# Performance work log

Measured on AMD Instinct MI355X. Metric: run time of the kernel, lower is better.

## Reference

```python
import jax, jax.numpy as jnp
import numpy as np

EPS = 1e-5
CHUNK = 512  # chunk of known points for the running-argmin 1-NN search


def nn_idx(unknown, known):
    """1-NN index of each unknown point into known. unknown (B,n,3), known (B,m,3) -> (B,n) int32."""
    B, n, _ = unknown.shape
    m = known.shape[1]
    u2 = jnp.sum(unknown * unknown, axis=-1)  # (B,n)
    # (num_chunks, B, CHUNK, 3)
    kc = known.reshape(B, m // CHUNK, CHUNK, 3).transpose(1, 0, 2, 3)

    def step(carry, kch):
        best_d, best_i, off = carry
        k2 = jnp.sum(kch * kch, axis=-1)  # (B,CHUNK)
        # squared distances for this chunk: (B,n,CHUNK)
        d = u2[:, :, None] - 2.0 * jnp.einsum('bnd,bcd->bnc', unknown, kch) + k2[:, None, :]
        dmin = jnp.min(d, axis=-1)
        imin = jnp.argmin(d, axis=-1).astype(jnp.int32) + off
        upd = dmin < best_d
        return (jnp.where(upd, dmin, best_d), jnp.where(upd, imin, best_i), off + CHUNK), None

    init = (jnp.full((B, n), jnp.inf, unknown.dtype),
            jnp.zeros((B, n), jnp.int32),
            jnp.int32(0))
    (_, best_i, _), _ = jax.lax.scan(step, init, kc)
    return best_i


def bn_relu(x, gamma, beta):
    """Training-mode BatchNorm over (B, n) per channel followed by ReLU. x: (B,C,n)."""
    mean = jnp.mean(x, axis=(0, 2), keepdims=True)
    var = jnp.mean(jnp.square(x - mean), axis=(0, 2), keepdims=True)  # biased, as torch BN
    y = (x - mean) * jax.lax.rsqrt(var + EPS)
    return jax.nn.relu(y * gamma[None, :, None] + beta[None, :, None])


def setup_inputs() -> dict:
    key = jax.random.key(0)
    ks = jax.random.split(key, 8)
    B, n, m, C1, C2 = 2, 65536, 16384, 128, 256
    mlp = [C2 + C1, 256, 128]
    return {
        'unknown': jax.random.normal(ks[0], (B, n, 3), jnp.float32),
        'known': jax.random.normal(ks[1], (B, m, 3), jnp.float32),
        'unknow_feats': jax.random.normal(ks[2], (B, C1, n), jnp.float32),
        'known_feats': jax.random.normal(ks[3], (B, C2, m), jnp.float32),
        'w1': jax.random.normal(ks[4], (mlp[1], mlp[0]), jnp.float32) * (1.0 / np.sqrt(mlp[0])),
        'gamma1': jnp.ones((mlp[1],), jnp.float32),
        'beta1': jnp.zeros((mlp[1],), jnp.float32),
        'w2': jax.random.normal(ks[5], (mlp[2], mlp[1]), jnp.float32) * (1.0 / np.sqrt(mlp[1])),
        'gamma2': jnp.ones((mlp[2],), jnp.float32),
        'beta2': jnp.zeros((mlp[2],), jnp.float32),
    }


def reference(unknown, known, unknow_feats, known_feats, w1, gamma1, beta1, w2, gamma2, beta2):
    idx = nn_idx(unknown, known)  # (B,n) int32
    # gather: (B,C2,m) indexed along m -> (B,C2,n)
    interpolated = jnp.take_along_axis(known_feats, idx[:, None, :], axis=2)
    new_features = jnp.concatenate([interpolated, unknow_feats], axis=1)  # (B,C1+C2,n)
    h = bn_relu(jnp.einsum('oc,bcn->bon', w1, new_features), gamma1, beta1)
    out = bn_relu(jnp.einsum('oc,bcn->bon', w2, h), gamma2, beta2)
    return out  # (B, mlp[-1], n)
```

## Files before the change

kernel.cpp:

```cpp
#include <hip/hip_runtime.h>

typedef unsigned short u16;
typedef unsigned int u32;
typedef __bf16 bf16x8 __attribute__((ext_vector_type(8)));
typedef _Float16 f16;
typedef _Float16 f16x8 __attribute__((ext_vector_type(8)));
typedef float f32x4 __attribute__((ext_vector_type(4)));
typedef float f32x16 __attribute__((ext_vector_type(16)));

#define B_ 2
#define N_ 65536
#define M_ 16384
#define C1_ 128
#define C2_ 256
#define K1_ 384
#define O1_ 256
#define O2_ 128
#define JT_ 512
#define HT_ (JT_/2)
#define EPS2_ 131.072f
#define TFIN_ 8.0f

__device__ __forceinline__ u16 f2bf(float f) {
    u32 u = __float_as_uint(f);
    u32 r = (u + 0x7FFFu + ((u >> 16) & 1u)) >> 16;
    return (u16)r;
}
__device__ __forceinline__ float bf2f(u16 h) {
    return __uint_as_float(((u32)h) << 16);
}
__device__ __forceinline__ u32 pack2(float lo, float hi) {
    return (u32)f2bf(lo) | ((u32)f2bf(hi) << 16);
}
__device__ __forceinline__ uint4 pack8(float4 a, float4 b) {
    uint4 r;
    r.x = pack2(a.x, a.y); r.y = pack2(a.z, a.w);
    r.z = pack2(b.x, b.y); r.w = pack2(b.z, b.w);
    return r;
}
__device__ __forceinline__ u16 h2u(f16 h) {
    union { f16 h; u16 u; } c; c.h = h; return c.u;
}

__device__ __forceinline__ float mul_rn(float a, float b) {
    float p = __fmul_rn(a, b);
    asm volatile("" : "+v"(p));
    return p;
}
__device__ __forceinline__ float sq3_np(float x, float y, float z) {
    return __fadd_rn(__fadd_rn(mul_rn(x, x), mul_rn(y, y)), mul_rn(z, z));
}
__device__ __forceinline__ float dot3_fma(float a0, float b0, float a1, float b1,
                                          float a2, float b2) {
    return fmaf(a2, b2, fmaf(a1, b1, mul_rn(a0, b0)));
}


__global__ __launch_bounds__(256) void k_prep_u(const float* __restrict__ unk,
                                                u16* __restrict__ Aprep) {
    int g = blockIdx.x * 256 + threadIdx.x;
    const float* up = unk + (size_t)g * 3;
    float tx = -512.f * up[0], ty = -512.f * up[1], tz = -512.f * up[2];
    f16 xh = (f16)tx; f16 xl = (f16)(tx - (float)xh);
    f16 yh = (f16)ty; f16 yl = (f16)(ty - (float)yh);
    f16 zh = (f16)tz; f16 zl = (f16)(tz - (float)zh);
    u16 lo[8] = {h2u(xh), h2u(xh), h2u(xl), h2u(yh), h2u(yh), h2u(yl), h2u(zh), h2u(zh)};
    u16 hi[8] = {h2u(zl), 0x5C00u, 0x5C00u, 0, 0, 0, 0, 0};
    u16* tb = Aprep + ((size_t)(g >> 5)) * 512;
    int r = g & 31;
    *(uint4*)(tb + r * 8) = *(uint4*)lo;
    *(uint4*)(tb + (r + 32) * 8) = *(uint4*)hi;
}

__global__ __launch_bounds__(256) void k_prep_k(const float* __restrict__ kn,
                                                u16* __restrict__ Bprep,
                                                float4* __restrict__ kco) {
    int g = blockIdx.x * 256 + threadIdx.x;
    const float* kp = kn + (size_t)g * 3;
    float x = kp[0], y = kp[1], z = kp[2];
    float qv = sq3_np(x, y, z);
    float sx = 256.f * x, sy = 256.f * y, sz = 256.f * z, sq = 256.f * qv;
    f16 xh = (f16)sx; f16 xl = (f16)(sx - (float)xh);
    f16 yh = (f16)sy; f16 yl = (f16)(sy - (float)yh);
    f16 zh = (f16)sz; f16 zl = (f16)(sz - (float)zh);
    f16 qh = (f16)sq; f16 ql = (f16)(sq - (float)qh);
    u16 lo[8] = {h2u(xh), h2u(xl), h2u(xh), h2u(yh), h2u(yl), h2u(yh), h2u(zh), h2u(zl)};
    u16 hi[8] = {h2u(zh), h2u(qh), h2u(ql), 0x5C00u, 0x5C00u, 0, 0, 0};
    u16* tb = Bprep + ((size_t)(g >> 5)) * 512;
    int r = g & 31;
    *(uint4*)(tb + r * 8) = *(uint4*)lo;
    *(uint4*)(tb + (r + 32) * 8) = *(uint4*)hi;
    kco[g] = make_float4(x, y, z, qv);
}

__global__ __launch_bounds__(256, 4) void k_nn(
        const u16* __restrict__ Aprep, const u16* __restrict__ Bprep,
        const float* __restrict__ unk, const float4* __restrict__ kco,
        unsigned long long* __restrict__ pc) {
    __shared__ unsigned long long cand[256];
    __shared__ float thrS[256];
    const int t = threadIdx.x;
    const int half = blockIdx.y, b = blockIdx.z;
    const int lane = t & 63, w = t >> 6;
    const int rowbase = blockIdx.x * 256;
    const u16* at = Aprep + (((size_t)(b * N_ + rowbase + w * 64)) >> 5) * 512;
    f16x8 af0 = *(const f16x8*)(at + lane * 8);
    f16x8 af1 = *(const f16x8*)(at + 512 + lane * 8);
    const u16* Bp = Bprep + ((size_t)b * JT_ + (size_t)half * HT_) * 512 + lane * 8;
    cand[t] = ~0ULL;

    const f32x16 zz = {0.f,0.f,0.f,0.f,0.f,0.f,0.f,0.f,0.f,0.f,0.f,0.f,0.f,0.f,0.f,0.f};

    f32x16 rm0, rm1;
#pragma unroll
    for (int r = 0; r < 16; ++r) { rm0[r] = 3.4e38f; rm1[r] = 3.4e38f; }

    f16x8 c0 = *(const f16x8*)Bp;
    f16x8 c1 = *(const f16x8*)(Bp + 512);
    for (int tp = 0; tp < HT_; tp += 2) {
        f16x8 n0 = *(const f16x8*)(Bp + 1024);
        f16x8 n1 = *(const f16x8*)(Bp + 1536);
        Bp += 1024;
        f32x16 a  = __builtin_amdgcn_mfma_f32_32x32x16_f16(af0, c0, zz, 0, 0, 0);
        f32x16 ca = __builtin_amdgcn_mfma_f32_32x32x16_f16(af0, c1, zz, 0, 0, 0);
#pragma unroll
        for (int r = 0; r < 16; ++r)
            rm0[r] = fminf(fminf(rm0[r], a[r]), ca[r]);
        a  = __builtin_amdgcn_mfma_f32_32x32x16_f16(af1, c0, zz, 0, 0, 0);
        ca = __builtin_amdgcn_mfma_f32_32x32x16_f16(af1, c1, zz, 0, 0, 0);
#pragma unroll
        for (int r = 0; r < 16; ++r)
            rm1[r] = fminf(fminf(rm1[r], a[r]), ca[r]);
        c0 = n0; c1 = n1;
    }

#pragma unroll
    for (int r = 0; r < 16; ++r) {
        float v0 = rm0[r], v1 = rm1[r];
        v0 = fminf(v0, __shfl_xor(v0, 1));  v1 = fminf(v1, __shfl_xor(v1, 1));
        v0 = fminf(v0, __shfl_xor(v0, 2));  v1 = fminf(v1, __shfl_xor(v1, 2));
        v0 = fminf(v0, __shfl_xor(v0, 4));  v1 = fminf(v1, __shfl_xor(v1, 4));
        v0 = fminf(v0, __shfl_xor(v0, 8));  v1 = fminf(v1, __shfl_xor(v1, 8));
        v0 = fminf(v0, __shfl_xor(v0, 16)); v1 = fminf(v1, __shfl_xor(v1, 16));
        if ((lane & 31) == 0) {
            int rl = w * 64 + ((lane >> 5) << 2) + (r & 3) + 8 * (r >> 2);
            thrS[rl] = v0 + EPS2_;
            thrS[rl + 32] = v1 + EPS2_;
        }
    }
    if (lane >= 32) {
        float tf0 = (thrS[w * 64 + (lane & 31)] + TFIN_) * 0.00390625f;
        f16 h0 = (f16)(-tf0);
        af0[3] = h0; af0[4] = (f16)(-tf0 - (float)h0);
        float tf1 = (thrS[w * 64 + 32 + (lane & 31)] + TFIN_) * 0.00390625f;
        f16 h1 = (f16)(-tf1);
        af1[3] = h1; af1[4] = (f16)(-tf1 - (float)h1);
    }

    const float4* kcb = kco + (size_t)b * M_;
    const float* ub = unk + (size_t)b * N_ * 3;
    const int rloc0 = w * 64 + ((lane >> 5) << 2);
    const int jb0 = half * (M_ / 2);

#define REFINE(RL, AV)                                                         \
    if ((AV) <= 0.f) {                                                         \
        int rl = (RL);                                                         \
        const float* up = ub + (size_t)(rowbase + rl) * 3;                     \
        float x = up[0], y = up[1], zc = up[2];                                \
        float uq = sq3_np(x, y, zc);                                           \
        float dot = dot3_fma(x, kc.x, y, kc.y, zc, kc.z);                      \
        float d = __fadd_rn(fmaf(-2.0f, dot, uq), kc.w);                       \
        u32 db = __float_as_uint(d);                                           \
        db = (db & 0x80000000u) ? ~db : (db | 0x80000000u);                    \
        atomicMin(&cand[rl], ((unsigned long long)db << 32) | (u32)j);         \
    }

    Bp -= (size_t)HT_ * 512;
    c0 = *(const f16x8*)Bp;
    f16x8 c1b = *(const f16x8*)(Bp + 512);
    for (int tt = 0; tt < HT_; ++tt) {
        f16x8 nx = *(const f16x8*)(Bp + 1024);
        Bp += 512;
        f32x16 a0 = __builtin_amdgcn_mfma_f32_32x32x16_f16(af0, c0, zz, 0, 0, 0);
        f32x16 a1 = __builtin_amdgcn_mfma_f32_32x32x16_f16(af1, c0, zz, 0, 0, 0);
        float gm0[4], gm1[4];
#pragma unroll
        for (int g = 0; g < 4; ++g) {
            gm0[g] = fminf(fminf(a0[4*g], a0[4*g+1]), fminf(a0[4*g+2], a0[4*g+3]));
            gm1[g] = fminf(fminf(a1[4*g], a1[4*g+1]), fminf(a1[4*g+2], a1[4*g+3]));
        }
        float gall = fminf(fminf(fminf(gm0[0], gm0[1]), fminf(gm0[2], gm0[3])),
                           fminf(fminf(gm1[0], gm1[1]), fminf(gm1[2], gm1[3])));
        if (__ballot(gall <= 0.f)) {
            int j = jb0 + tt * 32 + (lane & 31);
            float4 kc = kcb[j];
#pragma unroll
            for (int g = 0; g < 4; ++g) {
                if (__any(gm0[g] <= 0.f)) {
#pragma unroll
                    for (int rr = 0; rr < 4; ++rr)
                        REFINE(rloc0 + 8 * g + rr, a0[4*g+rr])
                }
                if (__any(gm1[g] <= 0.f)) {
#pragma unroll
                    for (int rr = 0; rr < 4; ++rr)
                        REFINE(rloc0 + 32 + 8 * g + rr, a1[4*g+rr])
                }
            }
        }
        c0 = c1b; c1b = nx;
    }
#undef REFINE
    pc[((size_t)(half * B_ + b)) * N_ + rowbase + t] = cand[t];
}

__global__ __launch_bounds__(256) void k_nn_merge(
        const unsigned long long* __restrict__ pc, int* __restrict__ idx) {
    int g = blockIdx.x * 256 + threadIdx.x;
    unsigned long long a = pc[g];
    unsigned long long c = pc[(size_t)(B_ * N_) + g];
    idx[g] = (int)(u32)((c < a ? c : a) & 0xFFFFFFFFu);
}

__global__ __launch_bounds__(256) void k_tr_kf(const float* __restrict__ kf,
                                               u16* __restrict__ kfT) {
    __shared__ float lt[64][65];
    const int t = threadIdx.x, b = blockIdx.z;
    const int j0 = blockIdx.x * 64, c0 = blockIdx.y * 64;
    const int jl = t & 63, cl4 = t >> 6;
#pragma unroll
    for (int p = 0; p < 16; ++p) {
        int c = c0 + cl4 + p * 4;
        lt[cl4 + p * 4][jl] = kf[((size_t)(b * C2_ + c)) * M_ + j0 + jl];
    }
    __syncthreads();
    const int cl = t & 63, jr4 = t >> 6;
#pragma unroll
    for (int p = 0; p < 16; ++p) {
        int j = j0 + jr4 + p * 4;
        kfT[((size_t)(b * M_ + j)) * C2_ + c0 + cl] = f2bf(lt[cl][jr4 + p * 4]);
    }
}

__global__ __launch_bounds__(256) void k_tr_uf(const float* __restrict__ uf,
                                               u16* __restrict__ newF) {
    __shared__ float lt[64][65];
    const int t = threadIdx.x, b = blockIdx.z;
    const int i0 = blockIdx.x * 64, c0 = blockIdx.y * 64;
    const int il = t & 63, cl4 = t >> 6;
#pragma unroll
    for (int p = 0; p < 16; ++p) {
        int c = c0 + cl4 + p * 4;
        lt[cl4 + p * 4][il] = uf[((size_t)(b * C1_ + c)) * N_ + i0 + il];
    }
    __syncthreads();
    const int cl = t & 63, ir4 = t >> 6;
#pragma unroll
    for (int p = 0; p < 16; ++p) {
        int i = i0 + ir4 + p * 4;
        newF[((size_t)(b * N_ + i)) * K1_ + C2_ + c0 + cl] = f2bf(lt[cl][ir4 + p * 4]);
    }
}

__global__ __launch_bounds__(256) void k_gather(const u16* __restrict__ kfT,
                                                const int* __restrict__ idx,
                                                u16* __restrict__ newF) {
    const int t = threadIdx.x, b = blockIdx.y;
    const int il = t >> 5, qq = t & 31;
    const int i = blockIdx.x * 8 + il;
    const int j = idx[b * N_ + i];
    const uint4* src = (const uint4*)(kfT + ((size_t)(b * M_ + j)) * C2_) + qq;
    uint4* dst = (uint4*)(newF + ((size_t)(b * N_ + i)) * K1_) + qq;
    *dst = *src;
}

__global__ __launch_bounds__(256) void k_gemm1(const u16* __restrict__ newF,
                                               const float* __restrict__ w1,
                                               u16* __restrict__ y1,
                                               float* __restrict__ bsum,
                                               float* __restrict__ bsq) {
    __shared__ u16 As[128 * 40];
    __shared__ u16 Bs[128 * 40];
    const int t = threadIdx.x, b = blockIdx.z;
    const int i0 = blockIdx.x * 128, o0 = blockIdx.y * 128;
    const int lane = t & 63, wv = t >> 6, wr = wv >> 1, wc = wv & 1;
    const int col = lane & 15, q = lane >> 4;

    const int rA0 = t >> 2, sA0 = t & 3;
    const u16* aS0 = newF + ((size_t)(b * N_ + i0 + rA0)) * K1_ + sA0 * 8;
    const u16* aS1 = aS0 + (size_t)64 * K1_;
    const float* bS0 = w1 + (size_t)(o0 + rA0) * K1_ + sA0 * 8;
    const float* bS1 = bS0 + (size_t)64 * K1_;
    u16* aD0 = &As[rA0 * 40 + sA0 * 8];
    u16* aD1 = aD0 + 64 * 40;
    u16* bD0 = &Bs[rA0 * 40 + sA0 * 8];
    u16* bD1 = bD0 + 64 * 40;

    f32x4 acc[4][4];
#pragma unroll
    for (int m = 0; m < 4; ++m)
#pragma unroll
        for (int n = 0; n < 4; ++n) acc[m][n] = (f32x4){0.f, 0.f, 0.f, 0.f};

    uint4 a0 = *(const uint4*)aS0, a1 = *(const uint4*)aS1;
    float4 f00 = *(const float4*)bS0, f01 = *(const float4*)(bS0 + 4);
    float4 f10 = *(const float4*)bS1, f11 = *(const float4*)(bS1 + 4);

    for (int ks = 0; ks < 12; ++ks) {
        __syncthreads();
        *(uint4*)aD0 = a0; *(uint4*)aD1 = a1;
        *(uint4*)bD0 = pack8(f00, f01); *(uint4*)bD1 = pack8(f10, f11);
        __syncthreads();
        if (ks < 11) {
            int ko = (ks + 1) * 32;
            a0 = *(const uint4*)(aS0 + ko); a1 = *(const uint4*)(aS1 + ko);
            f00 = *(const float4*)(bS0 + ko); f01 = *(const float4*)(bS0 + ko + 4);
            f10 = *(const float4*)(bS1 + ko); f11 = *(const float4*)(bS1 + ko + 4);
        }
        const u16* ap = &As[(wr * 64 + col) * 40 + q * 8];
        const u16* bp = &Bs[(wc * 64 + col) * 40 + q * 8];
        bf16x8 af[4], bfr[4];
#pragma unroll
        for (int m = 0; m < 4; ++m) af[m] = *(const bf16x8*)(ap + m * 640);
#pragma unroll
        for (int n = 0; n < 4; ++n) bfr[n] = *(const bf16x8*)(bp + n * 640);
#pragma unroll
        for (int m = 0; m < 4; ++m)
#pragma unroll
            for (int n = 0; n < 4; ++n)
                acc[m][n] = __builtin_amdgcn_mfma_f32_16x16x32_bf16(af[m], bfr[n], acc[m][n], 0, 0, 0);
    }
    float ssum[4], ssq[4];
#pragma unroll
    for (int n = 0; n < 4; ++n) { ssum[n] = 0.f; ssq[n] = 0.f; }
#pragma unroll
    for (int m = 0; m < 4; ++m)
#pragma unroll
        for (int n = 0; n < 4; ++n) {
            int go = o0 + wc * 64 + n * 16 + col;
#pragma unroll
            for (int r = 0; r < 4; ++r) {
                int gi = i0 + wr * 64 + m * 16 + q * 4 + r;
                u16 hv = f2bf(acc[m][n][r]);
                y1[((size_t)(b * N_ + gi)) * O1_ + go] = hv;
                float v = bf2f(hv);
                ssum[n] += v; ssq[n] = fmaf(v, v, ssq[n]);
            }
        }
#pragma unroll
    for (int n = 0; n < 4; ++n) {
        float s = ssum[n], qv = ssq[n];
        s += __shfl_xor(s, 16); qv += __shfl_xor(qv, 16);
        s += __shfl_xor(s, 32); qv += __shfl_xor(qv, 32);
        if (q == 0) {
            int go = o0 + wc * 64 + n * 16 + col;
            atomicAdd(&bsum[go], s);
            atomicAdd(&bsq[go], qv);
        }
    }
}

__global__ void k_bn_fin(const float* __restrict__ sum, const float* __restrict__ sq,
                         const float* __restrict__ gamma, const float* __restrict__ beta,
                         float* __restrict__ scale, float* __restrict__ bias,
                         int C, float invN) {
    int t = threadIdx.x;
    if (t < C) {
        float mean = sum[t] * invN;
        float var = sq[t] * invN - mean * mean;
        float rs = rsqrtf(var + 1e-5f);
        float sc = gamma[t] * rs;
        scale[t] = sc;
        bias[t] = beta[t] - mean * sc;
    }
}

__global__ __launch_bounds__(256) void k_gemm2(const u16* __restrict__ y1,
                                               const float* __restrict__ w2,
                                               const float* __restrict__ s1,
                                               const float* __restrict__ b1,
                                               float* __restrict__ y2,
                                               float* __restrict__ bsum,
                                               float* __restrict__ bsq) {
    __shared__ u16 As[128 * 40];
    __shared__ u16 Bs[128 * 40];
    const int t = threadIdx.x, b = blockIdx.z;
    const int i0 = blockIdx.x * 128;
    const int lane = t & 63, wv = t >> 6, wr = wv >> 1, wc = wv & 1;
    const int col = lane & 15, q = lane >> 4;

    const int rA0 = t >> 2, sA0 = t & 3;
    const u16* aS0 = y1 + ((size_t)(b * N_ + i0 + rA0)) * O1_ + sA0 * 8;
    const u16* aS1 = aS0 + (size_t)64 * O1_;
    const float* bS0 = w2 + (size_t)rA0 * O1_ + sA0 * 8;
    const float* bS1 = bS0 + (size_t)64 * O1_;
    u16* aD0 = &As[rA0 * 40 + sA0 * 8];
    u16* aD1 = aD0 + 64 * 40;
    u16* bD0 = &Bs[rA0 * 40 + sA0 * 8];
    u16* bD1 = bD0 + 64 * 40;

    f32x4 acc[4][4];
#pragma unroll
    for (int m = 0; m < 4; ++m)
#pragma unroll
        for (int n = 0; n < 4; ++n) acc[m][n] = (f32x4){0.f, 0.f, 0.f, 0.f};

    uint4 a0 = *(const uint4*)aS0, a1 = *(const uint4*)aS1;
    float4 f00 = *(const float4*)bS0, f01 = *(const float4*)(bS0 + 4);
    float4 f10 = *(const float4*)bS1, f11 = *(const float4*)(bS1 + 4);

    for (int ks = 0; ks < 8; ++ks) {
        int oc = ks * 32 + sA0 * 8;
        float4 sc0 = *(const float4*)(s1 + oc), sc1 = *(const float4*)(s1 + oc + 4);
        float4 bb0 = *(const float4*)(b1 + oc), bb1 = *(const float4*)(b1 + oc + 4);
        uint4 h0, h1;
        {
            const u16* hs = (const u16*)&a0;
            float v[8];
            v[0] = fmaxf(fmaf(bf2f(hs[0]), sc0.x, bb0.x), 0.f);
            v[1] = fmaxf(fmaf(bf2f(hs[1]), sc0.y, bb0.y), 0.f);
            v[2] = fmaxf(fmaf(bf2f(hs[2]), sc0.z, bb0.z), 0.f);
            v[3] = fmaxf(fmaf(bf2f(hs[3]), sc0.w, bb0.w), 0.f);
            v[4] = fmaxf(fmaf(bf2f(hs[4]), sc1.x, bb1.x), 0.f);
            v[5] = fmaxf(fmaf(bf2f(hs[5]), sc1.y, bb1.y), 0.f);
            v[6] = fmaxf(fmaf(bf2f(hs[6]), sc1.z, bb1.z), 0.f);
            v[7] = fmaxf(fmaf(bf2f(hs[7]), sc1.w, bb1.w), 0.f);
            h0.x = pack2(v[0], v[1]); h0.y = pack2(v[2], v[3]);
            h0.z = pack2(v[4], v[5]); h0.w = pack2(v[6], v[7]);
        }
        {
            const u16* hs = (const u16*)&a1;
            float v[8];
            v[0] = fmaxf(fmaf(bf2f(hs[0]), sc0.x, bb0.x), 0.f);
            v[1] = fmaxf(fmaf(bf2f(hs[1]), sc0.y, bb0.y), 0.f);
            v[2] = fmaxf(fmaf(bf2f(hs[2]), sc0.z, bb0.z), 0.f);
            v[3] = fmaxf(fmaf(bf2f(hs[3]), sc0.w, bb0.w), 0.f);
            v[4] = fmaxf(fmaf(bf2f(hs[4]), sc1.x, bb1.x), 0.f);
            v[5] = fmaxf(fmaf(bf2f(hs[5]), sc1.y, bb1.y), 0.f);
            v[6] = fmaxf(fmaf(bf2f(hs[6]), sc1.z, bb1.z), 0.f);
            v[7] = fmaxf(fmaf(bf2f(hs[7]), sc1.w, bb1.w), 0.f);
            h1.x = pack2(v[0], v[1]); h1.y = pack2(v[2], v[3]);
            h1.z = pack2(v[4], v[5]); h1.w = pack2(v[6], v[7]);
        }
        __syncthreads();
        *(uint4*)aD0 = h0; *(uint4*)aD1 = h1;
        *(uint4*)bD0 = pack8(f00, f01); *(uint4*)bD1 = pack8(f10, f11);
        __syncthreads();
        if (ks < 7) {
            int ko = (ks + 1) * 32;
            a0 = *(const uint4*)(aS0 + ko); a1 = *(const uint4*)(aS1 + ko);
            f00 = *(const float4*)(bS0 + ko); f01 = *(const float4*)(bS0 + ko + 4);
            f10 = *(const float4*)(bS1 + ko); f11 = *(const float4*)(bS1 + ko + 4);
        }
        const u16* ap = &As[(wr * 64 + col) * 40 + q * 8];
        const u16* bp = &Bs[(wc * 64 + col) * 40 + q * 8];
        bf16x8 af[4], bfr[4];
#pragma unroll
        for (int m = 0; m < 4; ++m) af[m] = *(const bf16x8*)(ap + m * 640);
#pragma unroll
        for (int n = 0; n < 4; ++n) bfr[n] = *(const bf16x8*)(bp + n * 640);
#pragma unroll
        for (int m = 0; m < 4; ++m)
#pragma unroll
            for (int n = 0; n < 4; ++n)
                acc[m][n] = __builtin_amdgcn_mfma_f32_16x16x32_bf16(af[m], bfr[n], acc[m][n], 0, 0, 0);
    }
    float ssum[4], ssq[4];
#pragma unroll
    for (int n = 0; n < 4; ++n) { ssum[n] = 0.f; ssq[n] = 0.f; }
#pragma unroll
    for (int m = 0; m < 4; ++m)
#pragma unroll
        for (int n = 0; n < 4; ++n) {
            int go = wc * 64 + n * 16 + col;
#pragma unroll
            for (int r = 0; r < 4; ++r) {
                int gi = i0 + wr * 64 + m * 16 + q * 4 + r;
                float v = acc[m][n][r];
                y2[((size_t)(b * N_ + gi)) * O2_ + go] = v;
                ssum[n] += v; ssq[n] = fmaf(v, v, ssq[n]);
            }
        }
#pragma unroll
    for (int n = 0; n < 4; ++n) {
        float s = ssum[n], qv = ssq[n];
        s += __shfl_xor(s, 16); qv += __shfl_xor(qv, 16);
        s += __shfl_xor(s, 32); qv += __shfl_xor(qv, 32);
        if (q == 0) {
            int go = wc * 64 + n * 16 + col;
            atomicAdd(&bsum[go], s);
            atomicAdd(&bsq[go], qv);
        }
    }
}

__global__ __launch_bounds__(256) void k_out(const float* __restrict__ y2,
                                             const float* __restrict__ s2,
                                             const float* __restrict__ b2,
                                             float* __restrict__ out) {
    __shared__ float lt[64 * 65];
    const int t = threadIdx.x, b = blockIdx.z;
    const int i0 = blockIdx.x * 64, o0 = blockIdx.y * 64;
    const int oc = t & 63, ir4 = t >> 6;
    const float sc = s2[o0 + oc], bs = b2[o0 + oc];
#pragma unroll
    for (int p = 0; p < 16; ++p) {
        int i = i0 + ir4 + p * 4;
        float v = y2[((size_t)(b * N_ + i)) * O2_ + o0 + oc];
        lt[oc * 65 + ir4 + p * 4] = fmaxf(fmaf(v, sc, bs), 0.f);
    }
    __syncthreads();
    const int il = t & 63, or4 = t >> 6;
#pragma unroll
    for (int p = 0; p < 16; ++p) {
        int o = o0 + or4 + p * 4;
        out[((size_t)(b * O2_ + o)) * N_ + i0 + il] = lt[(or4 + p * 4) * 65 + il];
    }
}

extern "C" void kernel_launch(void* const* d_in, const int* in_sizes, int n_in,
                              void* d_out, int out_size, void* d_ws, size_t ws_size,
                              hipStream_t stream) {
    const float* unknown = (const float*)d_in[0];
    const float* known   = (const float*)d_in[1];
    const float* uf      = (const float*)d_in[2];
    const float* kf      = (const float*)d_in[3];
    const float* w1      = (const float*)d_in[4];
    const float* g1      = (const float*)d_in[5];
    const float* be1     = (const float*)d_in[6];
    const float* w2      = (const float*)d_in[7];
    const float* g2      = (const float*)d_in[8];
    const float* be2     = (const float*)d_in[9];
    float* out = (float*)d_out;

    char* w = (char*)d_ws;
    float* bn1_sum = (float*)w;
    float* bn1_sq  = bn1_sum + 256;
    float* bn2_sum = bn1_sq + 256;
    float* bn2_sq  = bn2_sum + 128;
    float* s1 = (float*)(w + 4096);
    float* b1 = s1 + 256;
    float* s2 = b1 + 256;
    float* b2 = s2 + 128;
    int* idx = (int*)(w + 8192);
    u16* newF = (u16*)(w + 532480);
    float* y2 = (float*)(w + 532480);
    size_t R2 = 532480 + 100663296ULL;
    u16*   Aprep = (u16*)(w + R2);
    u16*   Bprep = (u16*)(w + R2 + 4194304ULL);
    float4* kco  = (float4*)(w + R2 + 5242880ULL);
    unsigned long long* pc = (unsigned long long*)(w + R2 + 5767168ULL);
    u16*  kfT = (u16*)(w + R2 + 16777216ULL);
    u16*   y1 = (u16*)(w + R2);

    hipMemsetAsync(w, 0, 3072, stream);

    k_prep_u<<<512, 256, 0, stream>>>(unknown, Aprep);
    k_prep_k<<<128, 256, 0, stream>>>(known, Bprep, kco);
    k_nn<<<dim3(N_ / 256, 2, B_), 256, 0, stream>>>(Aprep, Bprep, unknown, kco, pc);
    k_nn_merge<<<512, 256, 0, stream>>>(pc, idx);
    k_tr_kf<<<dim3(256, 4, 2), 256, 0, stream>>>(kf, kfT);
    k_tr_uf<<<dim3(1024, 2, 2), 256, 0, stream>>>(uf, newF);
    k_gather<<<dim3(8192, 2), 256, 0, stream>>>(kfT, idx, newF);
    k_gemm1<<<dim3(512, 2, 2), 256, 0, stream>>>(newF, w1, y1, bn1_sum, bn1_sq);
    k_bn_fin<<<1, 256, 0, stream>>>(bn1_sum, bn1_sq, g1, be1, s1, b1, 256, 1.f / 131072.f);
    k_gemm2<<<dim3(512, 1, 2), 256, 0, stream>>>(y1, w2, s1, b1, y2, bn2_sum, bn2_sq);
    k_bn_fin<<<1, 256, 0, stream>>>(bn2_sum, bn2_sq, g2, be2, s2, b2, 128, 1.f / 131072.f);
    k_out<<<dim3(1024, 2, 2), 256, 0, stream>>>(y2, s2, b2, out);
}
```

Before: 592.8 us.

## Fuse NN gather into GEMM1 and drop split-half NN merge

The NN search kernel now handles 128 rows per block over all known points, which removes the two-half split and the separate merge kernel. It caches unknown coordinates and norms in shared memory for the refine step and tests for candidates with a sign-bit OR instead of fmin chains. The gather kernel and the concatenated newF buffer are gone: GEMM1 reads gathered known features directly through idx, plus the transposed unknown features. This saves a large write and read of the intermediate but gives GEMM1 scattered row loads, and the NN kernel does twice the sequential work per block with half the rows per wave.

Measured after the change: 555.9 us. 6.2% less time.

```diff
diff --git a/kernel.cpp b/kernel.cpp
--- a/kernel.cpp
+++ b/kernel.cpp
@@ -17,7 +17,6 @@
 #define O1_ 256
 #define O2_ 128
 #define JT_ 512
-#define HT_ (JT_/2)
 #define EPS2_ 131.072f
 #define TFIN_ 8.0f
 
@@ -96,130 +95,120 @@
 __global__ __launch_bounds__(256, 4) void k_nn(
         const u16* __restrict__ Aprep, const u16* __restrict__ Bprep,
         const float* __restrict__ unk, const float4* __restrict__ kco,
-        unsigned long long* __restrict__ pc) {
-    __shared__ unsigned long long cand[256];
-    __shared__ float thrS[256];
-    const int t = threadIdx.x;
-    const int half = blockIdx.y, b = blockIdx.z;
+        int* __restrict__ idx) {
+    __shared__ unsigned long long cand[128];
+    __shared__ float thrS[128];
+    __shared__ float4 uS[128];
+    const int t = threadIdx.x, b = blockIdx.y;
     const int lane = t & 63, w = t >> 6;
-    const int rowbase = blockIdx.x * 256;
-    const u16* at = Aprep + (((size_t)(b * N_ + rowbase + w * 64)) >> 5) * 512;
-    f16x8 af0 = *(const f16x8*)(at + lane * 8);
-    f16x8 af1 = *(const f16x8*)(at + 512 + lane * 8);
-    const u16* Bp = Bprep + ((size_t)b * JT_ + (size_t)half * HT_) * 512 + lane * 8;
-    cand[t] = ~0ULL;
+    const int rowbase = blockIdx.x * 128;
+    const u16* at = Aprep + (((size_t)(b * N_ + rowbase + w * 32)) >> 5) * 512;
+    f16x8 af = *(const f16x8*)(at + lane * 8);
+    const u16* Bp = Bprep + ((size_t)b * JT_) * 512 + lane * 8;
+
+    if (t < 128) {
+        const float* up = unk + ((size_t)(b * N_ + rowbase + t)) * 3;
+        float x = up[0], y = up[1], z = up[2];
+        uS[t] = make_float4(x, y, z, sq3_np(x, y, z));
+        cand[t] = ~0ULL;
+    }
+    __syncthreads();
 
     const f32x16 zz = {0.f,0.f,0.f,0.f,0.f,0.f,0.f,0.f,0.f,0.f,0.f,0.f,0.f,0.f,0.f,0.f};
 
-    f32x16 rm0, rm1;
-#pragma unroll
-    for (int r = 0; r < 16; ++r) { rm0[r] = 3.4e38f; rm1[r] = 3.4e38f; }
+    f32x16 rm;
+#pragma unroll
+    for (int r = 0; r < 16; ++r) rm[r] = 3.4e38f;
 
     f16x8 c0 = *(const f16x8*)Bp;
     f16x8 c1 = *(const f16x8*)(Bp + 512);
-    for (int tp = 0; tp < HT_; tp += 2) {
+    for (int tp = 0; tp < JT_; tp += 2) {
         f16x8 n0 = *(const f16x8*)(Bp + 1024);
         f16x8 n1 = *(const f16x8*)(Bp + 1536);
         Bp += 1024;
-        f32x16 a  = __builtin_amdgcn_mfma_f32_32x32x16_f16(af0, c0, zz, 0, 0, 0);
-        f32x16 ca = __builtin_amdgcn_mfma_f32_32x32x16_f16(af0, c1, zz, 0, 0, 0);
+        f32x16 a  = __builtin_amdgcn_mfma_f32_32x32x16_f16(af, c0, zz, 0, 0, 0);
+        f32x16 ca = __builtin_amdgcn_mfma_f32_32x32x16_f16(af, c1, zz, 0, 0, 0);
 #pragma unroll
         for (int r = 0; r < 16; ++r)
-            rm0[r] = fminf(fminf(rm0[r], a[r]), ca[r]);
-        a  = __builtin_amdgcn_mfma_f32_32x32x16_f16(af1, c0, zz, 0, 0, 0);
-        ca = __builtin_amdgcn_mfma_f32_32x32x16_f16(af1, c1, zz, 0, 0, 0);
-#pragma unroll
-        for (int r = 0; r < 16; ++r)
-            rm1[r] = fminf(fminf(rm1[r], a[r]), ca[r]);
+            rm[r] = fminf(fminf(rm[r], a[r]), ca[r]);
         c0 = n0; c1 = n1;
     }
 
 #pragma unroll
     for (int r = 0; r < 16; ++r) {
-        float v0 = rm0[r], v1 = rm1[r];
-        v0 = fminf(v0, __shfl_xor(v0, 1));  v1 = fminf(v1, __shfl_xor(v1, 1));
-        v0 = fminf(v0, __shfl_xor(v0, 2));  v1 = fminf(v1, __shfl_xor(v1, 2));
-        v0 = fminf(v0, __shfl_xor(v0, 4));  v1 = fminf(v1, __shfl_xor(v1, 4));
-        v0 = fminf(v0, __shfl_xor(v0, 8));  v1 = fminf(v1, __shfl_xor(v1, 8));
-        v0 = fminf(v0, __shfl_xor(v0, 16)); v1 = fminf(v1, __shfl_xor(v1, 16));
+        float v = rm[r];
+        v = fminf(v, __shfl_xor(v, 1));
+        v = fminf(v, __shfl_xor(v, 2));
+        v = fminf(v, __shfl_xor(v, 4));
+        v = fminf(v, __shfl_xor(v, 8));
+        v = fminf(v, __shfl_xor(v, 16));
         if ((lane & 31) == 0) {
-            int rl = w * 64 + ((lane >> 5) << 2) + (r & 3) + 8 * (r >> 2);
-            thrS[rl] = v0 + EPS2_;
-            thrS[rl + 32] = v1 + EPS2_;
+            int rl = w * 32 + ((lane >> 5) << 2) + (r & 3) + 8 * (r >> 2);
+            thrS[rl] = v + EPS2_;
         }
     }
     if (lane >= 32) {
-        float tf0 = (thrS[w * 64 + (lane & 31)] + TFIN_) * 0.00390625f;
-        f16 h0 = (f16)(-tf0);
-        af0[3] = h0; af0[4] = (f16)(-tf0 - (float)h0);
-        float tf1 = (thrS[w * 64 + 32 + (lane & 31)] + TFIN_) * 0.00390625f;
-        f16 h1 = (f16)(-tf1);
-        af1[3] = h1; af1[4] = (f16)(-tf1 - (float)h1);
+        float tf = (thrS[w * 32 + (lane & 31)] + TFIN_) * 0.00390625f;
+        f16 h0 = (f16)(-tf);
+        af[3] = h0; af[4] = (f16)(-tf - (float)h0);
     }
 
     const float4* kcb = kco + (size_t)b * M_;
-    const float* ub = unk + (size_t)b * N_ * 3;
-    const int rloc0 = w * 64 + ((lane >> 5) << 2);
-    const int jb0 = half * (M_ / 2);
+    const int rloc0 = w * 32 + ((lane >> 5) << 2);
 
 #define REFINE(RL, AV)                                                         \
     if ((AV) <= 0.f) {                                                         \
         int rl = (RL);                                                         \
-        const float* up = ub + (size_t)(rowbase + rl) * 3;                     \
-        float x = up[0], y = up[1], zc = up[2];                                \
-        float uq = sq3_np(x, y, zc);                                           \
-        float dot = dot3_fma(x, kc.x, y, kc.y, zc, kc.z);                      \
-        float d = __fadd_rn(fmaf(-2.0f, dot, uq), kc.w);                       \
+        float4 uv = uS[rl];                                                    \
+        float dot = dot3_fma(uv.x, kc.x, uv.y, kc.y, uv.z, kc.z);              \
+        float d = __fadd_rn(fmaf(-2.0f, dot, uv.w), kc.w);                     \
         u32 db = __float_as_uint(d);                                           \
         db = (db & 0x80000000u) ? ~db : (db | 0x80000000u);                    \
         atomicMin(&cand[rl], ((unsigned long long)db << 32) | (u32)j);         \
     }
 
-    Bp -= (size_t)HT_ * 512;
+    Bp -= (size_t)JT_ * 512;
     c0 = *(const f16x8*)Bp;
     f16x8 c1b = *(const f16x8*)(Bp + 512);
-    for (int tt = 0; tt < HT_; ++tt) {
+    for (int tt = 0; tt < JT_; ++tt) {
         f16x8 nx = *(const f16x8*)(Bp + 1024);
         Bp += 512;
-        f32x16 a0 = __builtin_amdgcn_mfma_f32_32x32x16_f16(af0, c0, zz, 0, 0, 0);
-        f32x16 a1 = __builtin_amdgcn_mfma_f32_32x32x16_f16(af1, c0, zz, 0, 0, 0);
-        float gm0[4], gm1[4];
-#pragma unroll
-        for (int g = 0; g < 4; ++g) {
-            gm0[g] = fminf(fminf(a0[4*g], a0[4*g+1]), fminf(a0[4*g+2], a0[4*g+3]));
-            gm1[g] = fminf(fminf(a1[4*g], a1[4*g+1]), fminf(a1[4*g+2], a1[4*g+3]));
-        }
-        float gall = fminf(fminf(fminf(gm0[0], gm0[1]), fminf(gm0[2], gm0[3])),
-                           fminf(fminf(gm1[0], gm1[1]), fminf(gm1[2], gm1[3])));
-        if (__ballot(gall <= 0.f)) {
-            int j = jb0 + tt * 32 + (lane & 31);
+        f32x16 a = __builtin_amdgcn_mfma_f32_32x32x16_f16(af, c0, zz, 0, 0, 0);
+        u32 g0 = __float_as_uint(a[0]) | __float_as_uint(a[1])
+               | __float_as_uint(a[2]) | __float_as_uint(a[3]);
+        u32 g1 = __float_as_uint(a[4]) | __float_as_uint(a[5])
+               | __float_as_uint(a[6]) | __float_as_uint(a[7]);
+        u32 g2 = __float_as_uint(a[8]) | __float_as_uint(a[9])
+               | __float_as_uint(a[10]) | __float_as_uint(a[11]);
+        u32 g3 = __float_as_uint(a[12]) | __float_as_uint(a[13])
+               | __float_as_uint(a[14]) | __float_as_uint(a[15]);
+        u32 oall = g0 | g1 | g2 | g3;
+        if (__ballot((int)oall < 0)) {
+            int j = tt * 32 + (lane & 31);
             float4 kc = kcb[j];
-#pragma unroll
-            for (int g = 0; g < 4; ++g) {
-                if (__any(gm0[g] <= 0.f)) {
-#pragma unroll
-                    for (int rr = 0; rr < 4; ++rr)
-                        REFINE(rloc0 + 8 * g + rr, a0[4*g+rr])
-                }
-                if (__any(gm1[g] <= 0.f)) {
-#pragma unroll
-                    for (int rr = 0; rr < 4; ++rr)
-                        REFINE(rloc0 + 32 + 8 * g + rr, a1[4*g+rr])
-                }
+            if (__any((int)g0 < 0)) {
+#pragma unroll
+                for (int rr = 0; rr < 4; ++rr) REFINE(rloc0 + rr, a[rr])
+            }
+            if (__any((int)g1 < 0)) {
+#pragma unroll
+                for (int rr = 0; rr < 4; ++rr) REFINE(rloc0 + 8 + rr, a[4 + rr])
+            }
+            if (__any((int)g2 < 0)) {
+#pragma unroll
+                for (int rr = 0; rr < 4; ++rr) REFINE(rloc0 + 16 + rr, a[8 + rr])
+            }
+            if (__any((int)g3 < 0)) {
+#pragma unroll
+                for (int rr = 0; rr < 4; ++rr) REFINE(rloc0 + 24 + rr, a[12 + rr])
             }
         }
         c0 = c1b; c1b = nx;
     }
 #undef REFINE
-    pc[((size_t)(half * B_ + b)) * N_ + rowbase + t] = cand[t];
-}
-
-__global__ __launch_bounds__(256) void k_nn_merge(
-        const unsigned long long* __restrict__ pc, int* __restrict__ idx) {
-    int g = blockIdx.x * 256 + threadIdx.x;
-    unsigned long long a = pc[g];
-    unsigned long long c = pc[(size_t)(B_ * N_) + g];
-    idx[g] = (int)(u32)((c < a ? c : a) & 0xFFFFFFFFu);
+    __syncthreads();
+    if (t < 128)
+        idx[b * N_ + rowbase + t] = (int)(u32)(cand[t] & 0xFFFFFFFFu);
 }
 
 __global__ __launch_bounds__(256) void k_tr_kf(const float* __restrict__ kf,
@@ -243,7 +232,7 @@
 }
 
 __global__ __launch_bounds__(256) void k_tr_uf(const float* __restrict__ uf,
-                                               u16* __restrict__ newF) {
+                                               u16* __restrict__ ufT) {
     __shared__ float lt[64][65];
     const int t = threadIdx.x, b = blockIdx.z;
     const int i0 = blockIdx.x * 64, c0 = blockIdx.y * 64;
@@ -258,23 +247,13 @@
 #pragma unroll
     for (int p = 0; p < 16; ++p) {
         int i = i0 + ir4 + p * 4;
-        newF[((size_t)(b * N_ + i)) * K1_ + C2_ + c0 + cl] = f2bf(lt[cl][ir4 + p * 4]);
-    }
-}
-
-__global__ __launch_bounds__(256) void k_gather(const u16* __restrict__ kfT,
-                                                const int* __restrict__ idx,
-                                                u16* __restrict__ newF) {
-    const int t = threadIdx.x, b = blockIdx.y;
-    const int il = t >> 5, qq = t & 31;
-    const int i = blockIdx.x * 8 + il;
-    const int j = idx[b * N_ + i];
-    const uint4* src = (const uint4*)(kfT + ((size_t)(b * M_ + j)) * C2_) + qq;
-    uint4* dst = (uint4*)(newF + ((size_t)(b * N_ + i)) * K1_) + qq;
-    *dst = *src;
-}
-
-__global__ __launch_bounds__(256) void k_gemm1(const u16* __restrict__ newF,
+        ufT[((size_t)(b * N_ + i)) * C1_ + c0 + cl] = f2bf(lt[cl][ir4 + p * 4]);
+    }
+}
+
+__global__ __launch_bounds__(256) void k_gemm1(const u16* __restrict__ kfT,
+                                               const u16* __restrict__ ufT,
+                                               const int* __restrict__ idx,
                                                const float* __restrict__ w1,
                                                u16* __restrict__ y1,
                                                float* __restrict__ bsum,
@@ -287,8 +266,12 @@
     const int col = lane & 15, q = lane >> 4;
 
     const int rA0 = t >> 2, sA0 = t & 3;
-    const u16* aS0 = newF + ((size_t)(b * N_ + i0 + rA0)) * K1_ + sA0 * 8;
-    const u16* aS1 = aS0 + (size_t)64 * K1_;
+    const int j0 = idx[b * N_ + i0 + rA0];
+    const int j1 = idx[b * N_ + i0 + 64 + rA0];
+    const u16* kA0 = kfT + ((size_t)(b * M_ + j0)) * C2_ + sA0 * 8;
+    const u16* kA1 = kfT + ((size_t)(b * M_ + j1)) * C2_ + sA0 * 8;
+    const u16* uA0 = ufT + ((size_t)(b * N_ + i0 + rA0)) * C1_ + sA0 * 8;
+    const u16* uA1 = uA0 + (size_t)64 * C1_;
     const float* bS0 = w1 + (size_t)(o0 + rA0) * K1_ + sA0 * 8;
     const float* bS1 = bS0 + (size_t)64 * K1_;
     u16* aD0 = &As[rA0 * 40 + sA0 * 8];
@@ -302,7 +285,7 @@
 #pragma unroll
         for (int n = 0; n < 4; ++n) acc[m][n] = (f32x4){0.f, 0.f, 0.f, 0.f};
 
-    uint4 a0 = *(const uint4*)aS0, a1 = *(const uint4*)aS1;
+    uint4 a0 = *(const uint4*)kA0, a1 = *(const uint4*)kA1;
     float4 f00 = *(const float4*)bS0, f01 = *(const float4*)(bS0 + 4);
     float4 f10 = *(const float4*)bS1, f11 = *(const float4*)(bS1 + 4);
 
@@ -312,8 +295,15 @@
         *(uint4*)bD0 = pack8(f00, f01); *(uint4*)bD1 = pack8(f10, f11);
         __syncthreads();
         if (ks < 11) {
-            int ko = (ks + 1) * 32;
-            a0 = *(const uint4*)(aS0 + ko); a1 = *(const uint4*)(aS1 + ko);
+            int kn = ks + 1;
+            if (kn < 8) {
+                a0 = *(const uint4*)(kA0 + kn * 32);
+                a1 = *(const uint4*)(kA1 + kn * 32);
+            } else {
+                a0 = *(const uint4*)(uA0 + (kn - 8) * 32);
+                a1 = *(const uint4*)(uA1 + (kn - 8) * 32);
+            }
+            int ko = kn * 32;
             f00 = *(const float4*)(bS0 + ko); f01 = *(const float4*)(bS0 + ko + 4);
             f10 = *(const float4*)(bS1 + ko); f11 = *(const float4*)(bS1 + ko + 4);
         }
@@ -543,26 +533,26 @@
     float* s2 = b1 + 256;
     float* b2 = s2 + 128;
     int* idx = (int*)(w + 8192);
-    u16* newF = (u16*)(w + 532480);
-    float* y2 = (float*)(w + 532480);
-    size_t R2 = 532480 + 100663296ULL;
-    u16*   Aprep = (u16*)(w + R2);
-    u16*   Bprep = (u16*)(w + R2 + 4194304ULL);
-    float4* kco  = (float4*)(w + R2 + 5242880ULL);
-    unsigned long long* pc = (unsigned long long*)(w + R2 + 5767168ULL);
-    u16*  kfT = (u16*)(w + R2 + 16777216ULL);
-    u16*   y1 = (u16*)(w + R2);
+    u16* ufT = (u16*)(w + 532480);
+    size_t A1 = 532480 + 33554432ULL;
+    u16* y1  = (u16*)(w + A1);
+    size_t A2 = A1 + 67108864ULL;
+    u16* kfT = (u16*)(w + A2);
+    size_t A3 = A2 + 16777216ULL;
+    u16* Aprep = (u16*)(w + A3);
+    u16* Bprep = (u16*)(w + A3 + 4194304ULL);
+    float4* kco = (float4*)(w + A3 + 5242880ULL);
+    size_t A4 = A3 + 5767168ULL;
+    float* y2 = (float*)(w + A4);
 
     hipMemsetAsync(w, 0, 3072, stream);
 
     k_prep_u<<<512, 256, 0, stream>>>(unknown, Aprep);
     k_prep_k<<<128, 256, 0, stream>>>(known, Bprep, kco);
-    k_nn<<<dim3(N_ / 256, 2, B_), 256, 0, stream>>>(Aprep, Bprep, unknown, kco, pc);
-    k_nn_merge<<<512, 256, 0, stream>>>(pc, idx);
+    k_nn<<<dim3(N_ / 128, B_), 256, 0, stream>>>(Aprep, Bprep, unknown, kco, idx);
     k_tr_kf<<<dim3(256, 4, 2), 256, 0, stream>>>(kf, kfT);
-    k_tr_uf<<<dim3(1024, 2, 2), 256, 0, stream>>>(uf, newF);
-    k_gather<<<dim3(8192, 2), 256, 0, stream>>>(kfT, idx, newF);
-    k_gemm1<<<dim3(512, 2, 2), 256, 0, stream>>>(newF, w1, y1, bn1_sum, bn1_sq);
+    k_tr_uf<<<dim3(1024, 2, 2), 256, 0, stream>>>(uf, ufT);
+    k_gemm1<<<dim3(512, 2, 2), 256, 0, stream>>>(kfT, ufT, idx, w1, y1, bn1_sum, bn1_sq);
     k_bn_fin<<<1, 256, 0, stream>>>(bn1_sum, bn1_sq, g1, be1, s1, b1, 256, 1.f / 131072.f);
     k_gemm2<<<dim3(512, 1, 2), 256, 0, stream>>>(y1, w2, s1, b1, y2, bn2_sum, bn2_sq);
     k_bn_fin<<<1, 256, 0, stream>>>(bn2_sum, bn2_sq, g2, be2, s2, b2, 128, 1.f / 131072.f);
```
